# Kernel optimization log

Measured on AMD Instinct MI355X. Metric: run time of the kernel, lower is better.

Reference implementation:

```python
import jax, jax.numpy as jnp
import numpy as np

EPS = 1e-05
NUM_HEADS = 16
NUM_KV_HEADS = 8
HEAD_DIM = 128


def rms_norm(x, w, eps=EPS):
    var = jnp.mean(x.astype(jnp.float32) ** 2, axis=-1, keepdims=True)
    rstd = jax.lax.rsqrt(var + eps).astype(x.dtype)
    return (x * rstd) * w


def apply_rotary(x, cos, sin):
    # x: [B, H, S, D]; cos/sin: [B, S, D//2] -> broadcast over heads
    c = cos[:, None, :, :]
    s = sin[:, None, :, :]
    x1 = x[..., ::2]
    x2 = x[..., 1::2]
    return jnp.concatenate([x1 * c - x2 * s, x1 * s + x2 * c], axis=-1)


def setup_inputs() -> dict:
    key = jax.random.key(0)
    ks = jax.random.split(key, 12)
    B, S, D = 2, 2048, 2048
    Dff = 8192
    Dkv = NUM_KV_HEADS * HEAD_DIM
    sc = 0.02
    return {
        "hidden_states": jax.random.normal(ks[0], (B, S, D), jnp.float32),
        "cos": jax.random.uniform(ks[1], (B, S, HEAD_DIM // 2), jnp.float32),
        "sin": jax.random.uniform(ks[2], (B, S, HEAD_DIM // 2), jnp.float32),
        "attention_mask": jnp.zeros((B, 1, S, S), jnp.float32),
        "wq": jax.random.normal(ks[3], (D, D), jnp.float32) * sc,
        "wk": jax.random.normal(ks[4], (D, Dkv), jnp.float32) * sc,
        "wv": jax.random.normal(ks[5], (D, Dkv), jnp.float32) * sc,
        "wo": jax.random.normal(ks[6], (D, D), jnp.float32) * sc,
        "w_gate": jax.random.normal(ks[7], (D, Dff), jnp.float32) * sc,
        "w_up": jax.random.normal(ks[8], (D, Dff), jnp.float32) * sc,
        "w_down": jax.random.normal(ks[9], (Dff, D), jnp.float32) * sc,
        "ln1_w": jnp.ones((D,), jnp.float32),
        "ln2_w": jnp.ones((D,), jnp.float32),
    }


def reference(hidden_states, cos, sin, attention_mask, wq, wk, wv, wo,
              w_gate, w_up, w_down, ln1_w, ln2_w):
    B, S, D = hidden_states.shape
    n_rep = NUM_HEADS // NUM_KV_HEADS
    scale = HEAD_DIM ** -0.5

    # --- attention block ---
    residual = hidden_states
    x = rms_norm(hidden_states, ln1_w)

    q = (x @ wq).reshape(B, S, NUM_HEADS, HEAD_DIM).transpose(0, 2, 1, 3)
    k = (x @ wk).reshape(B, S, NUM_KV_HEADS, HEAD_DIM).transpose(0, 2, 1, 3)
    v = (x @ wv).reshape(B, S, NUM_KV_HEADS, HEAD_DIM).transpose(0, 2, 1, 3)

    q = apply_rotary(q, cos, sin)
    k = apply_rotary(k, cos, sin)

    k = jnp.repeat(k, n_rep, axis=1)  # [B, H, S, D]
    v = jnp.repeat(v, n_rep, axis=1)

    scores = jnp.einsum('bhqd,bhkd->bhqk', q, k) * scale + attention_mask
    weights = jax.nn.softmax(scores.astype(jnp.float32), axis=-1).astype(q.dtype)
    attn = jnp.einsum('bhqk,bhkd->bhqd', weights, v)
    attn = attn.transpose(0, 2, 1, 3).reshape(B, S, D)
    attn = attn @ wo

    hidden_states = residual + attn

    # --- SwiGLU FFN block ---
    residual = hidden_states
    x = rms_norm(hidden_states, ln2_w)
    gate = jax.nn.silu(x @ w_gate)
    up = x @ w_up
    out = (gate * up) @ w_down
    return residual + out
```

## Files before the change

### kernel.cpp

```cpp
#include <hip/hip_runtime.h>
#include <stdint.h>

typedef unsigned short u16;
typedef unsigned int u32;
typedef short bf16x8 __attribute__((ext_vector_type(8)));
typedef float f32x4 __attribute__((ext_vector_type(4)));

#define AS_GLOBAL __attribute__((address_space(1)))
#define AS_LDS    __attribute__((address_space(3)))

__device__ __forceinline__ float bf2f(u16 h) {
  union { u32 u; float f; } v; v.u = ((u32)h) << 16; return v.f;
}
__device__ __forceinline__ u16 f2bf(float f) {
  union { float f; u32 u; } v; v.f = f;
  return (u16)((v.u + 0x7FFFu + ((v.u >> 16) & 1u)) >> 16);
}
__device__ __forceinline__ float scrub(float v, float mark) {
  return (v == v && fabsf(v) < 1e30f) ? v : mark;
}
__device__ __forceinline__ void gload16(const void* g, void* l) {
  __builtin_amdgcn_global_load_lds((const AS_GLOBAL u32*)g, (AS_LDS u32*)l, 16, 0, 0);
}

__global__ __launch_bounds__(256) void detect_kernel(const u16* __restrict__ hs, int* flagp) {
  __shared__ int cnt;
  if (threadIdx.x == 0) cnt = 0;
  __syncthreads();
  int sane = 0;
  #pragma unroll
  for (int j = 0; j < 4; j++) {
    const u16 v = hs[(threadIdx.x * 4 + j) * 2];
    const int e = (v >> 7) & 0xFF;
    sane += (e >= 0x60 && e <= 0x8E) ? 1 : 0;
  }
  atomicAdd(&cnt, sane);
  __syncthreads();
  if (threadIdx.x == 0) *flagp = (cnt < 600) ? 1 : 0;
}

__global__ void init_flag2_kernel(int* flag2p) { *flag2p = 0; }

__global__ __launch_bounds__(256) void detect_mask_kernel(
    const void* __restrict__ mask, int n, const int* __restrict__ flagp, int* flag2p) {
  const int f = *flagp;
  const size_t nq = (size_t)n * (f ? 4 : 2) / 16;
  u32 acc = 0;
  for (size_t i = blockIdx.x * 256 + threadIdx.x; i < nq; i += (size_t)gridDim.x * 256) {
    const uint4 v = ((const uint4*)mask)[i];
    acc |= v.x | v.y | v.z | v.w;
  }
  if (__ballot(acc != 0) != 0ull && (threadIdx.x & 63) == 0)
    atomicOr(flag2p, 1);
}

__global__ __launch_bounds__(256) void convert_kernel(
    const void* __restrict__ src, u16* __restrict__ dst, int n, const int* __restrict__ flagp) {
  const int f = *flagp;
  const int i = (blockIdx.x * 256 + threadIdx.x) * 4;
  if (i >= n) return;
  union { uint2 u; u16 s[4]; } o;
  if (f) {
    const float4 v = *(const float4*)((const float*)src + i);
    o.s[0] = f2bf(v.x); o.s[1] = f2bf(v.y); o.s[2] = f2bf(v.z); o.s[3] = f2bf(v.w);
  } else {
    o.u = *(const uint2*)((const u16*)src + i);
  }
  *(uint2*)(dst + i) = o.u;
}

__global__ __launch_bounds__(256) void rmsnorm_in_kernel(
    const void* __restrict__ xin, const u16* __restrict__ w,
    u16* __restrict__ out, u16* __restrict__ srccopy, const int* __restrict__ flagp)
{
  __shared__ float red[4];
  const int row = blockIdx.x, tid = threadIdx.x;
  const int f = *flagp;
  union { uint4 q; u16 s[8]; } uu;
  if (f) {
    const float* xr = (const float*)xin + (size_t)row * 2048 + tid * 8;
    const float4 a = *(const float4*)xr, b = *(const float4*)(xr + 4);
    const float t[8] = {a.x, a.y, a.z, a.w, b.x, b.y, b.z, b.w};
    #pragma unroll
    for (int j = 0; j < 8; j++) uu.s[j] = f2bf(t[j]);
  } else {
    uu.q = *(const uint4*)((const u16*)xin + (size_t)row * 2048 + tid * 8);
  }
  *(uint4*)(srccopy + (size_t)row * 2048 + tid * 8) = uu.q;
  float v[8];
  #pragma unroll
  for (int j = 0; j < 8; j++) v[j] = bf2f(uu.s[j]);
  float ss = 0.f;
  #pragma unroll
  for (int j = 0; j < 8; j++) ss += v[j] * v[j];
  #pragma unroll
  for (int o = 32; o; o >>= 1) ss += __shfl_xor(ss, o, 64);
  if ((tid & 63) == 0) red[tid >> 6] = ss;
  __syncthreads();
  float rstd = rsqrtf((red[0] + red[1] + red[2] + red[3]) * (1.0f / 2048.0f) + 1e-5f);
  rstd = bf2f(f2bf(rstd));
  union { uint4 q; u16 s[8]; } ww; ww.q = *(const uint4*)(w + tid * 8);
  union { uint4 q; u16 s[8]; } oo;
  #pragma unroll
  for (int j = 0; j < 8; j++) oo.s[j] = f2bf(scrub(v[j] * rstd * bf2f(ww.s[j]), 200.f));
  *(uint4*)(out + (size_t)row * 2048 + tid * 8) = oo.q;
}

__global__ __launch_bounds__(256) void rmsnorm_kernel(
    const u16* __restrict__ xin, const u16* __restrict__ w, u16* __restrict__ out)
{
  __shared__ float red[4];
  const int row = blockIdx.x, tid = threadIdx.x;
  const u16* xr = xin + (size_t)row * 2048 + tid * 8;
  union { uint4 q; u16 s[8]; } uu; uu.q = *(const uint4*)xr;
  float v[8];
  #pragma unroll
  for (int j = 0; j < 8; j++) v[j] = bf2f(uu.s[j]);
  float ss = 0.f;
  #pragma unroll
  for (int j = 0; j < 8; j++) ss += v[j] * v[j];
  #pragma unroll
  for (int o = 32; o; o >>= 1) ss += __shfl_xor(ss, o, 64);
  if ((tid & 63) == 0) red[tid >> 6] = ss;
  __syncthreads();
  float rstd = rsqrtf((red[0] + red[1] + red[2] + red[3]) * (1.0f / 2048.0f) + 1e-5f);
  rstd = bf2f(f2bf(rstd));
  union { uint4 q; u16 s[8]; } ww; ww.q = *(const uint4*)(w + tid * 8);
  union { uint4 q; u16 s[8]; } oo;
  #pragma unroll
  for (int j = 0; j < 8; j++) oo.s[j] = f2bf(scrub(v[j] * rstd * bf2f(ww.s[j]), 200.f));
  *(uint4*)(out + (size_t)row * 2048 + tid * 8) = oo.q;
}

__global__ __launch_bounds__(256) void transpose_kernel(
    const void* __restrict__ in, u16* __restrict__ out, int R, int C,
    const int* __restrict__ flagp)
{
  __shared__ u16 tile[32][33];
  const int f = *flagp;
  const int tx = threadIdx.x, ty = threadIdx.y;
  const int x = blockIdx.x * 32 + tx;
  const int y0 = blockIdx.y * 32;
  if (f) {
    #pragma unroll
    for (int j = ty; j < 32; j += 8) tile[j][tx] = f2bf(((const float*)in)[(size_t)(y0 + j) * C + x]);
  } else {
    #pragma unroll
    for (int j = ty; j < 32; j += 8) tile[j][tx] = ((const u16*)in)[(size_t)(y0 + j) * C + x];
  }
  __syncthreads();
  const int xo = y0 + tx, yo0 = blockIdx.x * 32;
  #pragma unroll
  for (int j = ty; j < 32; j += 8) out[(size_t)(yo0 + j) * R + xo] = tile[tx][j];
}

enum { EPI_STORE = 0, EPI_ADD = 1, EPI_SILU = 2, EPI_ADD_OUT = 3 };

template<int EPI>
__global__ __launch_bounds__(256, 2) void gemm_bt_kernel(
    const u16* __restrict__ A, const u16* __restrict__ Bt,
    void* Cout, const void* aux, int M, int N, int K,
    int gx, int gy, const int* __restrict__ flagp)
{
  __shared__ alignas(16) u16 As[128 * 32];
  __shared__ alignas(16) u16 Bs[128 * 32];
  const int tid = threadIdx.x;
  const int wid = tid >> 6, lane = tid & 63;
  const int lrow = lane & 15, quad = lane >> 4;

  const int bandh = ((gy & 15) == 0) ? 16 : gy;
  const int per = gx * bandh;
  const int band = blockIdx.x / per;
  const int wrem = blockIdx.x - band * per;
  const int by = band * bandh + (wrem % bandh);
  const int bx = wrem / bandh;
  const int m0 = by * 128, n0 = bx * 128;

  const int wm = (wid >> 1) * 64, wn = (wid & 1) * 64;

  const int r0 = tid >> 2, p0 = tid & 3, g0 = p0 ^ ((r0 >> 1) & 3);
  const int r1 = 64 + (tid >> 2), g1 = p0 ^ ((r1 >> 1) & 3);

  const u16* Ar0 = A + (size_t)(m0 + r0) * K + g0 * 8;
  const u16* Ar1 = A + (size_t)(m0 + r1) * K + g1 * 8;
  const u16* Br0 = Bt + (size_t)(n0 + r0) * K + g0 * 8;
  const u16* Br1 = Bt + (size_t)(n0 + r1) * K + g1 * 8;

  f32x4 acc[4][4] = {};

  for (int k0 = 0; k0 < K; k0 += 32) {
    __syncthreads();
    gload16(Ar0 + k0, &As[wid * 512]);
    gload16(Ar1 + k0, &As[2048 + wid * 512]);
    gload16(Br0 + k0, &Bs[wid * 512]);
    gload16(Br1 + k0, &Bs[2048 + wid * 512]);
    __syncthreads();

    bf16x8 af[4], bfm[4];
    #pragma unroll
    for (int mt = 0; mt < 4; mt++) {
      int r = wm + mt * 16 + lrow;
      int p = quad ^ ((r >> 1) & 3);
      af[mt] = *(const bf16x8*)&As[r * 32 + p * 8];
    }
    #pragma unroll
    for (int nt = 0; nt < 4; nt++) {
      int r = wn + nt * 16 + lrow;
      int p = quad ^ ((r >> 1) & 3);
      bfm[nt] = *(const bf16x8*)&Bs[r * 32 + p * 8];
    }
    #pragma unroll
    for (int mt = 0; mt < 4; mt++)
      #pragma unroll
      for (int nt = 0; nt < 4; nt++)
        acc[mt][nt] = __builtin_amdgcn_mfma_f32_16x16x32_bf16(af[mt], bfm[nt], acc[mt][nt], 0, 0, 0);
  }

  const int oflag = (EPI == EPI_ADD_OUT) ? *flagp : 0;
  #pragma unroll
  for (int mt = 0; mt < 4; mt++)
    #pragma unroll
    for (int nt = 0; nt < 4; nt++)
      #pragma unroll
      for (int i = 0; i < 4; i++) {
        const int row = m0 + wm + mt * 16 + quad * 4 + i;
        const int col = n0 + wn + nt * 16 + lrow;
        const size_t idx = (size_t)row * N + col;
        const float vv = acc[mt][nt][i];
        if (EPI == EPI_STORE) {
          ((u16*)Cout)[idx] = f2bf(scrub(vv, 300.f));
        } else if (EPI == EPI_ADD) {
          ((u16*)Cout)[idx] = f2bf(scrub(bf2f(((const u16*)aux)[idx]) + vv, 700.f));
        } else if (EPI == EPI_SILU) {
          float g = bf2f(((const u16*)aux)[idx]);
          g = fminf(fmaxf(g, -30.f), 30.f);
          const float s = g / (1.0f + __expf(-g));
          ((u16*)Cout)[idx] = f2bf(scrub(s * vv, 800.f));
        } else {
          const float r = scrub(bf2f(((const u16*)aux)[idx]) + vv, 1e6f);
          if (oflag) ((float*)Cout)[idx] = r;
          else       ((u16*)Cout)[idx] = f2bf(r);
        }
      }
}

__global__ __launch_bounds__(256) void rope_kernel(
    u16* qkv, const u16* __restrict__ cosb, const u16* __restrict__ sinb)
{
  const int gw = blockIdx.x * 4 + (threadIdx.x >> 6);
  const int lane = threadIdx.x & 63;
  const int h = gw % 24;
  const int t = gw / 24;
  u16* base = qkv + (size_t)t * 4096 + h * 128;
  const u32 x01 = *(const u32*)(base + 2 * lane);
  const float x1 = bf2f((u16)(x01 & 0xffff));
  const float x2 = bf2f((u16)(x01 >> 16));
  const float c = bf2f(cosb[t * 64 + lane]);
  const float s = bf2f(sinb[t * 64 + lane]);
  const u16 o1 = f2bf(x1 * c - x2 * s);
  const u16 o2 = f2bf(x1 * s + x2 * c);
  base[lane] = o1;
  base[64 + lane] = o2;
}

#define VSTR 80
__global__ __launch_bounds__(256, 2) void flash_attn_kernel(
    const u16* __restrict__ qkv, const u16* __restrict__ vT,
    const void* __restrict__ mask, u16* __restrict__ obuf,
    const int* __restrict__ flagp, const int* __restrict__ zerop)
{
  __shared__ alignas(16) u16 Kt[64 * 128];
  __shared__ alignas(16) u16 Vt[128 * VSTR];
  __shared__ alignas(16) u16 Ps[4 * 16 * 64];

  const int qt = blockIdx.x, h = blockIdx.y, b = blockIdx.z;
  const int tid = threadIdx.x;
  const int wid = tid >> 6, lane = tid & 63;
  const int lrow = lane & 15, quad = lane >> 4;
  const int kvh = h >> 1;
  const size_t tok0 = (size_t)b * 2048;
  const int has_mask = *zerop;
  const int mf32 = *flagp;

  bf16x8 qf[4];
  {
    const u16* qptr = qkv + (tok0 + qt * 64 + wid * 16 + lrow) * 4096 + h * 128 + quad * 8;
    #pragma unroll
    for (int kk = 0; kk < 4; kk++) qf[kk] = *(const bf16x8*)(qptr + kk * 32);
  }
  const u16* kbase = qkv + tok0 * 4096 + 2048 + kvh * 128;
  const u16* vbase = vT + (size_t)(kvh * 128) * 4096 + tok0;

  float mst[4] = {-1e30f, -1e30f, -1e30f, -1e30f};
  float lst[4] = {0.f, 0.f, 0.f, 0.f};
  f32x4 oacc[8] = {};
  const float scale = 0.08838834764831845f;

  for (int kt = 0; kt < 32; kt++) {
    __syncthreads();
    #pragma unroll
    for (int ii = 0; ii < 4; ii++) {
      const int rloc = wid * 16 + ii * 4 + (lane >> 4);
      const int ch = lane & 15;
      const int gch = ch ^ (rloc & 7);
      gload16(kbase + (size_t)(kt * 64 + rloc) * 4096 + gch * 8,
              &Kt[(wid * 16 + ii * 4) * 128]);
    }
    #pragma unroll
    for (int ii = 0; ii < 4; ii++) {
      const int ci = ii * 256 + tid;
      const int d = ci >> 3, c = ci & 7;
      const int pos = c ^ (d & 7);
      const uint4 v = *(const uint4*)(vbase + (size_t)d * 4096 + kt * 64 + c * 8);
      *(uint4*)&Vt[d * VSTR + pos * 8] = v;
    }
    __syncthreads();

    f32x4 sfr[4] = {};
    #pragma unroll
    for (int nt = 0; nt < 4; nt++) {
      const int r = nt * 16 + lrow;
      #pragma unroll
      for (int kk = 0; kk < 4; kk++) {
        bf16x8 kf = *(const bf16x8*)&Kt[r * 128 + (((kk * 4 + quad) ^ (r & 7)) << 3)];
        sfr[nt] = __builtin_amdgcn_mfma_f32_16x16x32_bf16(qf[kk], kf, sfr[nt], 0, 0, 0);
      }
    }
    if (has_mask) {
      #pragma unroll
      for (int nt = 0; nt < 4; nt++)
        #pragma unroll
        for (int i = 0; i < 4; i++) {
          const size_t midx = (tok0 + qt * 64 + wid * 16 + quad * 4 + i) * 2048
                              + kt * 64 + nt * 16 + lrow;
          const float mv = mf32 ? ((const float*)mask)[midx] : bf2f(((const u16*)mask)[midx]);
          sfr[nt][i] = fminf(fmaxf(sfr[nt][i] * scale + mv, -1e4f), 1e4f);
        }
    } else {
      #pragma unroll
      for (int nt = 0; nt < 4; nt++)
        #pragma unroll
        for (int i = 0; i < 4; i++)
          sfr[nt][i] = fminf(fmaxf(sfr[nt][i] * scale, -1e4f), 1e4f);
    }
    float alpha[4], mnew[4], rsum[4];
    #pragma unroll
    for (int i = 0; i < 4; i++) {
      float mx = fmaxf(fmaxf(sfr[0][i], sfr[1][i]), fmaxf(sfr[2][i], sfr[3][i]));
      #pragma unroll
      for (int o = 8; o; o >>= 1) mx = fmaxf(mx, __shfl_xor(mx, o, 64));
      mnew[i] = fmaxf(mst[i], mx);
      alpha[i] = __expf(mst[i] - mnew[i]);
      mst[i] = mnew[i];
      rsum[i] = 0.f;
    }
    #pragma unroll
    for (int nt = 0; nt < 4; nt++)
      #pragma unroll
      for (int i = 0; i < 4; i++) {
        const float p = __expf(sfr[nt][i] - mnew[i]);
        rsum[i] += p;
        const int row = quad * 4 + i;
        const int c = nt * 2 + (lrow >> 3);
        Ps[wid * 1024 + row * 64 + ((c ^ (row & 7)) << 3) + (lrow & 7)] = f2bf(p);
      }
    #pragma unroll
    for (int i = 0; i < 4; i++) {
      #pragma unroll
      for (int o = 8; o; o >>= 1) rsum[i] += __shfl_xor(rsum[i], o, 64);
      lst[i] = lst[i] * alpha[i] + rsum[i];
    }
    #pragma unroll
    for (int dt = 0; dt < 8; dt++)
      #pragma unroll
      for (int i = 0; i < 4; i++) oacc[dt][i] *= alpha[i];

    asm volatile("s_waitcnt lgkmcnt(0)" ::: "memory");
    #pragma unroll
    for (int kk = 0; kk < 2; kk++) {
      bf16x8 pf = *(const bf16x8*)&Ps[wid * 1024 + lrow * 64 + (((kk * 4 + quad) ^ (lrow & 7)) << 3)];
      #pragma unroll
      for (int dt = 0; dt < 8; dt++) {
        const int d = dt * 16 + lrow;
        bf16x8 vf = *(const bf16x8*)&Vt[d * VSTR + (((kk * 4 + quad) ^ (d & 7)) << 3)];
        oacc[dt] = __builtin_amdgcn_mfma_f32_16x16x32_bf16(pf, vf, oacc[dt], 0, 0, 0);
      }
    }
  }

  #pragma unroll
  for (int dt = 0; dt < 8; dt++)
    #pragma unroll
    for (int i = 0; i < 4; i++) {
      const size_t tok = tok0 + qt * 64 + wid * 16 + quad * 4 + i;
      obuf[tok * 2048 + h * 128 + dt * 16 + lrow] = f2bf(scrub(oacc[dt][i] / lst[i], 500.f));
    }
}

extern "C" void kernel_launch(void* const* d_in, const int* in_sizes, int n_in,
                              void* d_out, int out_size, void* d_ws, size_t ws_size,
                              hipStream_t stream) {
  (void)in_sizes; (void)n_in; (void)out_size; (void)ws_size;
  const void* hs   = d_in[0];
  const void* cosi = d_in[1];
  const void* sini = d_in[2];
  const void* mask = d_in[3];
  const void* wq   = d_in[4];
  const void* wk   = d_in[5];
  const void* wv   = d_in[6];
  const void* wo   = d_in[7];
  const void* wg   = d_in[8];
  const void* wu   = d_in[9];
  const void* wd   = d_in[10];
  const void* ln1  = d_in[11];
  const void* ln2  = d_in[12];

  char* ws = (char*)d_ws;
  int* flag  = (int*)ws;
  int* flag2 = (int*)(ws + 64);
  u16* ln1b  = (u16*)(ws + 4096);
  u16* ln2b  = (u16*)(ws + 16384);
  u16* cosb  = (u16*)(ws + (1u << 20));
  u16* sinb  = (u16*)(ws + (1u << 20) + (1u << 19));
  u16* hsb   = (u16*)(ws + (2u  << 20));
  u16* xn    = (u16*)(ws + (18u << 20));
  u16* qkv   = (u16*)(ws + (34u << 20));
  u16* abuf  = (u16*)(ws + (66u << 20));
  u16* wT    = (u16*)(ws + (82u << 20));
  u16* gbuf  = (u16*)(ws + (114u << 20));
  u16* vT    = gbuf;
  u16* x2n   = hsb;
  u16* h2    = xn;

  dim3 tb(32, 8);
  detect_kernel<<<1, 256, 0, stream>>>((const u16*)hs, flag);
  init_flag2_kernel<<<1, 1, 0, stream>>>(flag2);
  detect_mask_kernel<<<2048, 256, 0, stream>>>(mask, 8388608, flag, flag2);
  convert_kernel<<<256,  256, 0, stream>>>(cosi, cosb, 262144,  flag);
  convert_kernel<<<256,  256, 0, stream>>>(sini, sinb, 262144,  flag);
  convert_kernel<<<2,    256, 0, stream>>>(ln1,  ln1b, 2048,    flag);
  convert_kernel<<<2,    256, 0, stream>>>(ln2,  ln2b, 2048,    flag);
  rmsnorm_in_kernel<<<4096, 256, 0, stream>>>(hs, ln1b, xn, hsb, flag);
  transpose_kernel<<<dim3(64, 64), tb, 0, stream>>>(wq, wT, 2048, 2048, flag);
  transpose_kernel<<<dim3(32, 64), tb, 0, stream>>>(wk, wT + (size_t)2048 * 2048, 2048, 1024, flag);
  transpose_kernel<<<dim3(32, 64), tb, 0, stream>>>(wv, wT + (size_t)3072 * 2048, 2048, 1024, flag);
  gemm_bt_kernel<EPI_STORE><<<24 * 32, 256, 0, stream>>>(xn, wT, qkv, nullptr, 4096, 4096, 2048, 24, 32, flag);
  gemm_bt_kernel<EPI_STORE><<<32 * 8, 256, 0, stream>>>(wT + (size_t)3072 * 2048, xn, vT, nullptr, 1024, 4096, 2048, 32, 8, flag);
  rope_kernel<<<24576, 256, 0, stream>>>(qkv, cosb, sinb);
  flash_attn_kernel<<<dim3(32, 16, 2), 256, 0, stream>>>(qkv, vT, mask, abuf, flag, flag2);
  transpose_kernel<<<dim3(64, 64), tb, 0, stream>>>(wo, wT, 2048, 2048, flag);
  gemm_bt_kernel<EPI_ADD><<<16 * 32, 256, 0, stream>>>(abuf, wT, h2, hsb, 4096, 2048, 2048, 16, 32, flag);
  rmsnorm_kernel<<<4096, 256, 0, stream>>>(h2, ln2b, x2n);
  transpose_kernel<<<dim3(256, 64), tb, 0, stream>>>(wg, wT, 2048, 8192, flag);
  gemm_bt_kernel<EPI_STORE><<<64 * 32, 256, 0, stream>>>(x2n, wT, gbuf, nullptr, 4096, 8192, 2048, 64, 32, flag);
  transpose_kernel<<<dim3(256, 64), tb, 0, stream>>>(wu, wT, 2048, 8192, flag);
  gemm_bt_kernel<EPI_SILU><<<64 * 32, 256, 0, stream>>>(x2n, wT, gbuf, gbuf, 4096, 8192, 2048, 64, 32, flag);
  transpose_kernel<<<dim3(64, 256), tb, 0, stream>>>(wd, wT, 8192, 2048, flag);
  gemm_bt_kernel<EPI_ADD_OUT><<<16 * 32, 256, 0, stream>>>(gbuf, wT, d_out, h2, 4096, 2048, 8192, 16, 32, flag);
}
```

Baseline: 1.224 ms.

## Double GEMM K-tile to 64 and remap blocks per XCD for L2 locality

The bf16 GEMM kernel now stages 64-wide K slices per iteration instead of 32. This halves the number of barrier pairs and load rounds per output tile, and the LDS swizzle is adapted to 8 chunks per row. The block-to-tile mapping now splits the grid into 8 partitions, one per XCD via blockIdx&7, with 8x8 supertiles inside each partition so blocks sharing a die reuse A/B rows in its L2. The cost is doubled LDS per block (32KB), which could limit occupancy at 2 blocks/CU, and the tile mapping depends on the grid dimensions.

```diff
diff --git a/kernel.cpp b/kernel.cpp
--- a/kernel.cpp
+++ b/kernel.cpp
@@ -162,58 +162,83 @@
     void* Cout, const void* aux, int M, int N, int K,
     int gx, int gy, const int* __restrict__ flagp)
 {
-  __shared__ alignas(16) u16 As[128 * 32];
-  __shared__ alignas(16) u16 Bs[128 * 32];
+  __shared__ alignas(16) u16 As[128 * 64];
+  __shared__ alignas(16) u16 Bs[128 * 64];
   const int tid = threadIdx.x;
   const int wid = tid >> 6, lane = tid & 63;
   const int lrow = lane & 15, quad = lane >> 4;
 
-  const int bandh = ((gy & 15) == 0) ? 16 : gy;
-  const int per = gx * bandh;
-  const int band = blockIdx.x / per;
-  const int wrem = blockIdx.x - band * per;
-  const int by = band * bandh + (wrem % bandh);
-  const int bx = wrem / bandh;
+  int by, bx;
+  const int Pr = ((gy & 1) == 0) ? 2 : 1;
+  const int Pc = 8 / Pr;
+  if ((gx % Pc) == 0 && (gy % Pr) == 0) {
+    const int ph = gy / Pr, pw = gx / Pc;
+    const int xcd = blockIdx.x & 7, local = blockIdx.x >> 3;
+    const int pr = xcd / Pc, pc = xcd % Pc;
+    int by_l, bx_l;
+    if ((ph & 7) == 0 && (pw & 7) == 0) {
+      const int t = local >> 6, u = local & 63;
+      const int tpr = ph >> 3;
+      const int ty = t % tpr, tx = t / tpr;
+      by_l = ty * 8 + (u & 7);
+      bx_l = tx * 8 + (u >> 3);
+    } else {
+      by_l = local % ph;
+      bx_l = local / ph;
+    }
+    by = pr * ph + by_l;
+    bx = pc * pw + bx_l;
+  } else {
+    by = blockIdx.x % gy;
+    bx = blockIdx.x / gy;
+  }
   const int m0 = by * 128, n0 = bx * 128;
 
   const int wm = (wid >> 1) * 64, wn = (wid & 1) * 64;
 
-  const int r0 = tid >> 2, p0 = tid & 3, g0 = p0 ^ ((r0 >> 1) & 3);
-  const int r1 = 64 + (tid >> 2), g1 = p0 ^ ((r1 >> 1) & 3);
-
-  const u16* Ar0 = A + (size_t)(m0 + r0) * K + g0 * 8;
-  const u16* Ar1 = A + (size_t)(m0 + r1) * K + g1 * 8;
-  const u16* Br0 = Bt + (size_t)(n0 + r0) * K + g0 * 8;
-  const u16* Br1 = Bt + (size_t)(n0 + r1) * K + g1 * 8;
+  int arow[4], apos[4];
+  #pragma unroll
+  for (int ii = 0; ii < 4; ii++) {
+    const int s = (wid * 4 + ii) * 64 + lane;
+    arow[ii] = s >> 3;
+    apos[ii] = (s & 7) ^ (arow[ii] & 7);
+  }
 
   f32x4 acc[4][4] = {};
 
-  for (int k0 = 0; k0 < K; k0 += 32) {
+  for (int k0 = 0; k0 < K; k0 += 64) {
     __syncthreads();
-    gload16(Ar0 + k0, &As[wid * 512]);
-    gload16(Ar1 + k0, &As[2048 + wid * 512]);
-    gload16(Br0 + k0, &Bs[wid * 512]);
-    gload16(Br1 + k0, &Bs[2048 + wid * 512]);
+    #pragma unroll
+    for (int ii = 0; ii < 4; ii++)
+      gload16(A + (size_t)(m0 + arow[ii]) * K + k0 + apos[ii] * 8,
+              &As[(wid * 4 + ii) * 512]);
+    #pragma unroll
+    for (int ii = 0; ii < 4; ii++)
+      gload16(Bt + (size_t)(n0 + arow[ii]) * K + k0 + apos[ii] * 8,
+              &Bs[(wid * 4 + ii) * 512]);
     __syncthreads();
 
-    bf16x8 af[4], bfm[4];
-    #pragma unroll
-    for (int mt = 0; mt < 4; mt++) {
-      int r = wm + mt * 16 + lrow;
-      int p = quad ^ ((r >> 1) & 3);
-      af[mt] = *(const bf16x8*)&As[r * 32 + p * 8];
-    }
-    #pragma unroll
-    for (int nt = 0; nt < 4; nt++) {
-      int r = wn + nt * 16 + lrow;
-      int p = quad ^ ((r >> 1) & 3);
-      bfm[nt] = *(const bf16x8*)&Bs[r * 32 + p * 8];
-    }
-    #pragma unroll
-    for (int mt = 0; mt < 4; mt++)
-      #pragma unroll
-      for (int nt = 0; nt < 4; nt++)
-        acc[mt][nt] = __builtin_amdgcn_mfma_f32_16x16x32_bf16(af[mt], bfm[nt], acc[mt][nt], 0, 0, 0);
+    #pragma unroll
+    for (int ko = 0; ko < 2; ko++) {
+      bf16x8 af[4], bfm[4];
+      #pragma unroll
+      for (int mt = 0; mt < 4; mt++) {
+        const int r = wm + mt * 16 + lrow;
+        const int p = (ko * 4 + quad) ^ (r & 7);
+        af[mt] = *(const bf16x8*)&As[r * 64 + p * 8];
+      }
+      #pragma unroll
+      for (int nt = 0; nt < 4; nt++) {
+        const int r = wn + nt * 16 + lrow;
+        const int p = (ko * 4 + quad) ^ (r & 7);
+        bfm[nt] = *(const bf16x8*)&Bs[r * 64 + p * 8];
+      }
+      #pragma unroll
+      for (int mt = 0; mt < 4; mt++)
+        #pragma unroll
+        for (int nt = 0; nt < 4; nt++)
+          acc[mt][nt] = __builtin_amdgcn_mfma_f32_16x16x32_bf16(af[mt], bfm[nt], acc[mt][nt], 0, 0, 0);
+    }
   }
 
   const int oflag = (EPI == EPI_ADD_OUT) ? *flagp : 0;
```

Result: faster. 1.144 ms (-6.6%).
